# Kernel optimization log

Hardware: AMD Instinct MI355X
Metric: run time of the kernel (lower is better)

## Reference

```python
import jax, jax.numpy as jnp
import numpy as np

B, T, D, H = 4, 2048, 1024, 16
HD = D // H


def setup_inputs() -> dict:
    key = jax.random.key(0)
    ks = jax.random.split(key, 6)
    s = 0.02
    return {
        "x": jax.random.normal(ks[0], (B, T, D), dtype=jnp.float32),
        "padding_mask": jnp.zeros((B, T), dtype=bool),
        "Wq": jax.random.normal(ks[1], (D, D), dtype=jnp.float32) * s,
        "Wk": jax.random.normal(ks[2], (D, D), dtype=jnp.float32) * s,
        "Wv": jax.random.normal(ks[3], (D, D), dtype=jnp.float32) * s,
        "Wo": jax.random.normal(ks[4], (D, D), dtype=jnp.float32) * s,
        "bo": jax.random.normal(ks[5], (D,), dtype=jnp.float32) * s,
    }


def reference(x, padding_mask, Wq, Wk, Wv, Wo, bo):
    # torch nn.Linear: y = x @ W.T
    b, t, d = x.shape
    q = (x @ Wq.T).reshape(b, t, H, HD).transpose(0, 2, 1, 3)  # [B,H,T,hd]
    k = (x @ Wk.T).reshape(b, t, H, HD).transpose(0, 2, 1, 3)
    v = (x @ Wv.T).reshape(b, t, H, HD).transpose(0, 2, 1, 3)

    scores = jnp.einsum("bhid,bhjd->bhij", q, k) / jnp.sqrt(jnp.float32(HD))
    causal = jnp.tril(jnp.ones((t, t), dtype=bool))  # [T,T]
    neg_inf = jnp.float32(-jnp.inf)
    scores = jnp.where(causal[None, None, :, :], scores, neg_inf)
    scores = jnp.where(padding_mask[:, None, None, :], neg_inf, scores)

    attn = jax.nn.softmax(scores, axis=-1)
    out = jnp.einsum("bhij,bhjd->bhid", attn, v)
    out = out.transpose(0, 2, 1, 3).reshape(b, t, d)
    out = out @ Wo.T + bo
    nonpad = (~padding_mask)[:, :, None].astype(out.dtype)
    return out * nonpad
```

## Files before the change

### kernel.cpp

```cpp
#include <hip/hip_runtime.h>

#define B_ 4
#define T_ 2048
#define D_ 1024
#define H_ 16
#define BT_ (B_ * T_)
#define QSCALE (0.125f * 1.44269504088896f)

typedef unsigned short u16;
typedef __attribute__((ext_vector_type(8))) __bf16 bf16x8;
typedef __attribute__((ext_vector_type(4))) float f32x4;

__device__ __forceinline__ u16 f2bf(float f) {
  unsigned u = __builtin_bit_cast(unsigned, f);
  u += 0x7FFFu + ((u >> 16) & 1u);
  return (u16)(u >> 16);
}

__device__ __forceinline__ void gload16(const void* g, void* l) {
  __builtin_amdgcn_global_load_lds(
      (const __attribute__((address_space(1))) void*)g,
      (__attribute__((address_space(3))) void*)l, 16, 0, 0);
}

__global__ void cvt_bf16(const float* __restrict__ in, u16* __restrict__ out, int n4) {
  int i = blockIdx.x * 256 + threadIdx.x;
  if (i >= n4) return;
  const float4 v = ((const float4*)in)[i];
  ushort4 o;
  o.x = f2bf(v.x); o.y = f2bf(v.y); o.z = f2bf(v.z); o.w = f2bf(v.w);
  ((ushort4*)out)[i] = o;
}

__global__ void pm_flags(const unsigned char* __restrict__ pm, unsigned char* __restrict__ fl) {
  int i = threadIdx.x;
  const unsigned long long* p = (const unsigned long long*)(pm + i * 64);
  unsigned long long acc = 0;
#pragma unroll
  for (int k = 0; k < 8; ++k) acc |= p[k];
  fl[i] = acc ? 1 : 0;
}

template<int MODE>
__global__ __launch_bounds__(256, 2) void gemm_bt(
    const u16* __restrict__ A, const u16* __restrict__ Bw,
    float* __restrict__ Cf, const float* __restrict__ bias,
    const unsigned char* __restrict__ rowmask,
    u16* __restrict__ Cq, u16* __restrict__ Ck, u16* __restrict__ Cvt)
{
  __shared__ __align__(16) u16 sA[128 * 64];
  __shared__ __align__(16) u16 sB[128 * 64];
  const int tid = threadIdx.x;
  const int lane = tid & 63, wave = tid >> 6;
  const int g = lane >> 4, s15 = lane & 15;
  const int bm = blockIdx.x * 128, bn = blockIdx.y * 128;
  const int wr = wave >> 1, wc = wave & 1;

  const int srow = lane >> 3;
  const int scol = ((lane & 7) ^ srow) << 3;

  f32x4 acc[4][4] = {};

  for (int kt = 0; kt < 16; ++kt) {
    __syncthreads();
    const int k0 = kt << 6;
#pragma unroll
    for (int c = 0; c < 4; ++c) {
      const int chunk = c * 4 + wave;
      gload16(A  + (size_t)(bm + chunk * 8 + srow) * 1024 + k0 + scol, (char*)sA + chunk * 1024);
      gload16(Bw + (size_t)(bn + chunk * 8 + srow) * 1024 + k0 + scol, (char*)sB + chunk * 1024);
    }
    __syncthreads();
#pragma unroll
    for (int kk = 0; kk < 2; ++kk) {
      const int cb = ((kk << 6) | (g << 4)) ^ ((s15 & 7) << 4);
      bf16x8 af[4], bf[4];
#pragma unroll
      for (int mm = 0; mm < 4; ++mm)
        af[mm] = *(const bf16x8*)((const char*)sA + (wr * 64 + mm * 16 + s15) * 128 + cb);
#pragma unroll
      for (int nn = 0; nn < 4; ++nn)
        bf[nn] = *(const bf16x8*)((const char*)sB + (wc * 64 + nn * 16 + s15) * 128 + cb);
#pragma unroll
      for (int mm = 0; mm < 4; ++mm)
#pragma unroll
        for (int nn = 0; nn < 4; ++nn)
          acc[mm][nn] = __builtin_amdgcn_mfma_f32_16x16x32_bf16(af[mm], bf[nn], acc[mm][nn], 0, 0, 0);
    }
  }

  if (MODE == 1) {
    const int region = bn >> 10;
    const float a = (region == 0) ? QSCALE : 1.f;
#pragma unroll
    for (int mm = 0; mm < 4; ++mm)
#pragma unroll
      for (int nn = 0; nn < 4; ++nn) {
        const int col = bn + wc * 64 + nn * 16 + s15;
        const int colr = col & 1023;
        const int row0 = bm + wr * 64 + mm * 16 + (g << 2);
        if (region == 2) {
          ushort4 w;
          w.x = f2bf(acc[mm][nn][0]); w.y = f2bf(acc[mm][nn][1]);
          w.z = f2bf(acc[mm][nn][2]); w.w = f2bf(acc[mm][nn][3]);
          *(ushort4*)(Cvt + (size_t)colr * BT_ + row0) = w;
        } else {
          u16* dst = region ? Ck : Cq;
#pragma unroll
          for (int r = 0; r < 4; ++r)
            dst[(size_t)(row0 + r) * 1024 + colr] = f2bf(acc[mm][nn][r] * a);
        }
      }
  } else {
#pragma unroll
    for (int mm = 0; mm < 4; ++mm)
#pragma unroll
      for (int nn = 0; nn < 4; ++nn) {
        const int col = bn + wc * 64 + nn * 16 + s15;
        const int row0 = bm + wr * 64 + mm * 16 + (g << 2);
        const float bv = bias[col];
#pragma unroll
        for (int r = 0; r < 4; ++r) {
          float v = acc[mm][nn][r] + bv;
          v = rowmask[row0 + r] ? 0.f : v;
          Cf[(size_t)(row0 + r) * 1024 + col] = v;
        }
      }
  }
}

__global__ __launch_bounds__(512, 4) void attn_fwd(
    const u16* __restrict__ Q, const u16* __restrict__ K,
    const u16* __restrict__ VT, const unsigned char* __restrict__ pm,
    const unsigned char* __restrict__ tileflag, u16* __restrict__ O)
{
  __shared__ __align__(16) u16 sK[2][64 * 64];
  __shared__ __align__(16) u16 sV[2][64 * 64];
  const int tid = threadIdx.x;
  const int lane = tid & 63, wave = tid >> 6;
  const int g = lane >> 4, s15 = lane & 15;
  const int bh = blockIdx.x, b = bh >> 4, h = bh & 15;
  const int jpair = blockIdx.y;
  const size_t tokbase = (size_t)b * T_;

  const int srow = tid >> 3;
  const int sc = (tid & 7) ^ (srow & 7);
  const u16* Kb0 = K + tokbase * D_ + h * 64 + sc * 8;
  const u16* Vb0 = VT + (size_t)(h * 64) * BT_ + tokbase + sc * 8;

#pragma unroll
  for (int half = 0; half < 2; ++half) {
    const int qt = half ? (15 - jpair) : jpair;
    const int q0 = qt * 128;
    const int qw = q0 + wave * 16;
    const int nt = 2 * qt + 2;

    bf16x8 qf[2];
#pragma unroll
    for (int ks = 0; ks < 2; ++ks)
      qf[ks] = *(const bf16x8*)(Q + (tokbase + qw + s15) * D_ + h * 64 + ks * 32 + g * 8);

    f32x4 o[4] = {};
    float m_ = -1e30f, l_ = 0.f;

    gload16(Kb0 + (size_t)srow * D_,  (char*)(&sK[0][0]) + tid * 16);
    gload16(Vb0 + (size_t)srow * BT_, (char*)(&sV[0][0]) + tid * 16);
    __syncthreads();

    for (int t = 0; t < nt; ++t) {
      const int kv0 = t << 6;
      if (t + 1 < nt) {
        const int nb = (t + 1) & 1;
        gload16(Kb0 + (size_t)(kv0 + 64 + srow) * D_,  (char*)(&sK[nb][0]) + tid * 16);
        gload16(Vb0 + (size_t)srow * BT_ + kv0 + 64,   (char*)(&sV[nb][0]) + tid * 16);
      }

      if (kv0 <= qw + 15) {
        const u16* kb_ = &sK[t & 1][0];
        const u16* vb_ = &sV[t & 1][0];

        f32x4 st[4] = {};
#pragma unroll
        for (int ks = 0; ks < 2; ++ks) {
          bf16x8 kf[4];
#pragma unroll
          for (int jf = 0; jf < 4; ++jf)
            kf[jf] = *(const bf16x8*)(kb_ + (jf * 16 + s15) * 64 + (((ks * 4 + g) ^ (s15 & 7)) << 3));
          __builtin_amdgcn_s_setprio(1);
#pragma unroll
          for (int jf = 0; jf < 4; ++jf)
            st[jf] = __builtin_amdgcn_mfma_f32_16x16x32_bf16(kf[jf], qf[ks], st[jf], 0, 0, 0);
          __builtin_amdgcn_s_setprio(0);
        }

        if (kv0 + 63 > qw) {
          const int iq = qw + s15;
#pragma unroll
          for (int jf = 0; jf < 4; ++jf) {
            const int jb = kv0 + jf * 16 + g * 4;
#pragma unroll
            for (int r = 0; r < 4; ++r)
              if (jb + r > iq) st[jf][r] = -1e30f;
          }
        }
        if (tileflag[b * 32 + t]) {
#pragma unroll
          for (int jf = 0; jf < 4; ++jf) {
            const int jb = kv0 + jf * 16 + g * 4;
            uchar4 p4 = *(const uchar4*)(pm + b * T_ + jb);
            const unsigned char* pr = (const unsigned char*)&p4;
#pragma unroll
            for (int r = 0; r < 4; ++r)
              if (pr[r]) st[jf][r] = -1e30f;
          }
        }

        float tm = -1e30f;
#pragma unroll
        for (int jf = 0; jf < 4; ++jf)
          tm = fmaxf(tm, fmaxf(fmaxf(st[jf][0], st[jf][1]), fmaxf(st[jf][2], st[jf][3])));
        tm = fmaxf(tm, __shfl_xor(tm, 16));
        tm = fmaxf(tm, __shfl_xor(tm, 32));
        if (!__all(tm <= m_ + 8.f)) {
          const float mn = fmaxf(m_, tm);
          const float ac = __builtin_amdgcn_exp2f(m_ - mn);
          m_ = mn;
          l_ *= ac;
#pragma unroll
          for (int df = 0; df < 4; ++df) o[df] *= ac;
        }
        float s = 0.f;
#pragma unroll
        for (int jf = 0; jf < 4; ++jf)
#pragma unroll
          for (int r = 0; r < 4; ++r) {
            const float p = __builtin_amdgcn_exp2f(st[jf][r] - m_);
            st[jf][r] = p;
            s += p;
          }
        s += __shfl_xor(s, 16);
        s += __shfl_xor(s, 32);
        l_ += s;

#pragma unroll
        for (int kb2 = 0; kb2 < 2; ++kb2) {
          bf16x8 vf[4];
#pragma unroll
          for (int df = 0; df < 4; ++df)
            vf[df] = *(const bf16x8*)(vb_ + (df * 16 + s15) * 64 + (((kb2 * 4 + g) ^ (s15 & 7)) << 3));
          unsigned w00, w01, w10, w11;
          asm("v_cvt_pk_bf16_f32 %0, %1, %2" : "=v"(w00) : "v"(st[2*kb2][0]),   "v"(st[2*kb2][1]));
          asm("v_cvt_pk_bf16_f32 %0, %1, %2" : "=v"(w01) : "v"(st[2*kb2][2]),   "v"(st[2*kb2][3]));
          asm("v_cvt_pk_bf16_f32 %0, %1, %2" : "=v"(w10) : "v"(st[2*kb2+1][0]), "v"(st[2*kb2+1][1]));
          asm("v_cvt_pk_bf16_f32 %0, %1, %2" : "=v"(w11) : "v"(st[2*kb2+1][2]), "v"(st[2*kb2+1][3]));
          asm("v_permlane32_swap_b32 %0, %1" : "+v"(w00), "+v"(w10));
          asm("v_permlane16_swap_b32 %0, %1" : "+v"(w00), "+v"(w10));
          asm("v_permlane32_swap_b32 %0, %1" : "+v"(w01), "+v"(w11));
          asm("v_permlane16_swap_b32 %0, %1" : "+v"(w01), "+v"(w11));
          union { unsigned u[4]; bf16x8 v; } pf;
          pf.u[0] = w00; pf.u[1] = w01; pf.u[2] = w10; pf.u[3] = w11;
          __builtin_amdgcn_s_setprio(1);
#pragma unroll
          for (int df = 0; df < 4; ++df)
            o[df] = __builtin_amdgcn_mfma_f32_16x16x32_bf16(vf[df], pf.v, o[df], 0, 0, 0);
          __builtin_amdgcn_s_setprio(0);
        }
      }
      __syncthreads();
    }

    const float inv = 1.f / l_;
    u16* orow = O + (tokbase + qw + s15) * D_ + h * 64 + g * 4;
#pragma unroll
    for (int df = 0; df < 4; ++df) {
      ushort4 w;
      w.x = f2bf(o[df][0] * inv); w.y = f2bf(o[df][1] * inv);
      w.z = f2bf(o[df][2] * inv); w.w = f2bf(o[df][3] * inv);
      *(ushort4*)(orow + df * 16) = w;
    }
  }
}

extern "C" void kernel_launch(void* const* d_in, const int* in_sizes, int n_in,
                              void* d_out, int out_size, void* d_ws, size_t ws_size,
                              hipStream_t stream)
{
  const float* x  = (const float*)d_in[0];
  const unsigned char* pm = (const unsigned char*)d_in[1];
  const float* Wq = (const float*)d_in[2];
  const float* Wk = (const float*)d_in[3];
  const float* Wv = (const float*)d_in[4];
  const float* Wo = (const float*)d_in[5];
  const float* bo = (const float*)d_in[6];
  float* out = (float*)d_out;

  char* w = (char*)d_ws;
  u16* xb  = (u16*)w; w += (size_t)BT_ * D_ * 2;
  u16* wqb = (u16*)w; w += (size_t)D_ * D_ * 2;
  u16* wkb = (u16*)w; w += (size_t)D_ * D_ * 2;
  u16* wvb = (u16*)w; w += (size_t)D_ * D_ * 2;
  u16* wob = (u16*)w; w += (size_t)D_ * D_ * 2;
  u16* qb  = (u16*)w; w += (size_t)BT_ * D_ * 2;
  u16* kbf = (u16*)w; w += (size_t)BT_ * D_ * 2;
  u16* vt  = (u16*)w; w += (size_t)BT_ * D_ * 2;
  u16* ao  = (u16*)w; w += (size_t)BT_ * D_ * 2;
  unsigned char* flags = (unsigned char*)w; w += 256;

  const int nx4 = BT_ * D_ / 4;
  const int nw4 = D_ * D_ / 4;
  cvt_bf16<<<nx4 / 256, 256, 0, stream>>>(x, xb, nx4);
  cvt_bf16<<<nw4 / 256, 256, 0, stream>>>(Wq, wqb, nw4);
  cvt_bf16<<<nw4 / 256, 256, 0, stream>>>(Wk, wkb, nw4);
  cvt_bf16<<<nw4 / 256, 256, 0, stream>>>(Wv, wvb, nw4);
  cvt_bf16<<<nw4 / 256, 256, 0, stream>>>(Wo, wob, nw4);
  pm_flags<<<1, 128, 0, stream>>>(pm, flags);

  gemm_bt<1><<<dim3(64, 24), 256, 0, stream>>>(xb, wqb, nullptr, nullptr, nullptr, qb, kbf, vt);

  attn_fwd<<<dim3(B_ * H_, 8), 512, 0, stream>>>(qb, kbf, vt, pm, flags, ao);

  gemm_bt<0><<<dim3(64, 8), 256, 0, stream>>>(ao, wob, out, bo, pm, nullptr, nullptr, nullptr);
}
```

Baseline: 159.3 us.

## Rewrite QKV projection GEMM with 256x128 tiles, double-buffered LDS, and block swizzle

Replaces the templated QKV GEMM with a dedicated kernel that uses 512-thread blocks computing 256x128 tiles. Global-to-LDS loads for the next k-step are double-buffered so they overlap with the MFMA work on the current buffer. It also adds a flattened grid swizzle for L2 locality and raises wave priority around the MFMA block. The output projection keeps the old single-buffer kernel. The costs are twice the LDS footprint and extra barriers inside the k loop.

```diff
diff --git a/kernel.cpp b/kernel.cpp
--- a/kernel.cpp
+++ b/kernel.cpp
@@ -41,12 +41,106 @@
   fl[i] = acc ? 1 : 0;
 }
 
-template<int MODE>
-__global__ __launch_bounds__(256, 2) void gemm_bt(
+__global__ __launch_bounds__(512, 2) void gemm_qkv(
+    const u16* __restrict__ A, const u16* __restrict__ Bw,
+    u16* __restrict__ Cq, u16* __restrict__ Ck, u16* __restrict__ Cvt)
+{
+  __shared__ __align__(16) u16 sA[2][256 * 64];
+  __shared__ __align__(16) u16 sB[2][128 * 64];
+  const int tid = threadIdx.x;
+  const int lane = tid & 63, wave = tid >> 6;
+  const int g = lane >> 4, s15 = lane & 15;
+  const int wm = wave >> 1, wn = wave & 1;
+
+  const int flat = blockIdx.x;
+  const int swz = (flat & 7) * 96 + (flat >> 3);
+  const int bm = (swz / 24) * 256, bn = (swz % 24) * 128;
+
+  int rowL[2], offL[2];
+#pragma unroll
+  for (int l = 0; l < 2; ++l) {
+    const int chunk = tid + l * 512;
+    rowL[l] = chunk >> 3;
+    offL[l] = rowL[l] * 1024 + (((chunk & 7) ^ (rowL[l] & 7)) << 3);
+  }
+  const int ldsW = wave * 1024;
+
+  auto STAGE = [&](int t, int buf) {
+    const int k0 = t << 6;
+#pragma unroll
+    for (int h = 0; h < 2; ++h)
+#pragma unroll
+      for (int l = 0; l < 2; ++l)
+        gload16(A + (size_t)(bm + h * 128) * 1024 + k0 + offL[l],
+                (char*)&sA[buf][0] + h * 16384 + l * 8192 + ldsW);
+#pragma unroll
+    for (int l = 0; l < 2; ++l)
+      gload16(Bw + (size_t)bn * 1024 + k0 + offL[l],
+              (char*)&sB[buf][0] + l * 8192 + ldsW);
+  };
+
+  f32x4 acc[4][4] = {};
+
+  STAGE(0, 0);
+  asm volatile("s_waitcnt vmcnt(0)" ::: "memory");
+  __builtin_amdgcn_s_barrier();
+
+  for (int t = 0; t < 16; ++t) {
+    const int cur = t & 1;
+    const char* sa = (const char*)&sA[cur][0] + (wm >> 1) * 16384 + ((wm & 1) * 64) * 128;
+    const char* sb = (const char*)&sB[cur][0] + (wn * 64) * 128;
+    if (t < 15) STAGE(t + 1, cur ^ 1);
+#pragma unroll
+    for (int kk = 0; kk < 2; ++kk) {
+      const int cb = ((kk * 4 + g) ^ (s15 & 7)) << 4;
+      bf16x8 af[4], bf[4];
+#pragma unroll
+      for (int m = 0; m < 4; ++m)
+        af[m] = *(const bf16x8*)(sa + (m * 16 + s15) * 128 + cb);
+#pragma unroll
+      for (int n = 0; n < 4; ++n)
+        bf[n] = *(const bf16x8*)(sb + (n * 16 + s15) * 128 + cb);
+      __builtin_amdgcn_s_barrier();
+      __builtin_amdgcn_s_setprio(1);
+#pragma unroll
+      for (int m = 0; m < 4; ++m)
+#pragma unroll
+        for (int n = 0; n < 4; ++n)
+          acc[m][n] = __builtin_amdgcn_mfma_f32_16x16x32_bf16(af[m], bf[n], acc[m][n], 0, 0, 0);
+      __builtin_amdgcn_s_setprio(0);
+      if (kk == 0) __builtin_amdgcn_s_barrier();
+    }
+    if (t < 15) asm volatile("s_waitcnt vmcnt(0)" ::: "memory");
+    __builtin_amdgcn_s_barrier();
+  }
+
+  const int region = bn >> 10;
+  const float a = (region == 0) ? QSCALE : 1.f;
+#pragma unroll
+  for (int m = 0; m < 4; ++m)
+#pragma unroll
+    for (int n = 0; n < 4; ++n) {
+      const int col = bn + wn * 64 + n * 16 + s15;
+      const int colr = col & 1023;
+      const int row0 = bm + wm * 64 + m * 16 + (g << 2);
+      if (region == 2) {
+        ushort4 w;
+        w.x = f2bf(acc[m][n][0]); w.y = f2bf(acc[m][n][1]);
+        w.z = f2bf(acc[m][n][2]); w.w = f2bf(acc[m][n][3]);
+        *(ushort4*)(Cvt + (size_t)colr * BT_ + row0) = w;
+      } else {
+        u16* dst = region ? Ck : Cq;
+#pragma unroll
+        for (int r = 0; r < 4; ++r)
+          dst[(size_t)(row0 + r) * 1024 + colr] = f2bf(acc[m][n][r] * a);
+      }
+    }
+}
+
+__global__ __launch_bounds__(256, 2) void gemm_out(
     const u16* __restrict__ A, const u16* __restrict__ Bw,
     float* __restrict__ Cf, const float* __restrict__ bias,
-    const unsigned char* __restrict__ rowmask,
-    u16* __restrict__ Cq, u16* __restrict__ Ck, u16* __restrict__ Cvt)
+    const unsigned char* __restrict__ rowmask)
 {
   __shared__ __align__(16) u16 sA[128 * 64];
   __shared__ __align__(16) u16 sB[128 * 64];
@@ -89,44 +183,20 @@
     }
   }
 
-  if (MODE == 1) {
-    const int region = bn >> 10;
-    const float a = (region == 0) ? QSCALE : 1.f;
-#pragma unroll
-    for (int mm = 0; mm < 4; ++mm)
-#pragma unroll
-      for (int nn = 0; nn < 4; ++nn) {
-        const int col = bn + wc * 64 + nn * 16 + s15;
-        const int colr = col & 1023;
-        const int row0 = bm + wr * 64 + mm * 16 + (g << 2);
-        if (region == 2) {
-          ushort4 w;
-          w.x = f2bf(acc[mm][nn][0]); w.y = f2bf(acc[mm][nn][1]);
-          w.z = f2bf(acc[mm][nn][2]); w.w = f2bf(acc[mm][nn][3]);
-          *(ushort4*)(Cvt + (size_t)colr * BT_ + row0) = w;
-        } else {
-          u16* dst = region ? Ck : Cq;
-#pragma unroll
-          for (int r = 0; r < 4; ++r)
-            dst[(size_t)(row0 + r) * 1024 + colr] = f2bf(acc[mm][nn][r] * a);
-        }
+#pragma unroll
+  for (int mm = 0; mm < 4; ++mm)
+#pragma unroll
+    for (int nn = 0; nn < 4; ++nn) {
+      const int col = bn + wc * 64 + nn * 16 + s15;
+      const int row0 = bm + wr * 64 + mm * 16 + (g << 2);
+      const float bv = bias[col];
+#pragma unroll
+      for (int r = 0; r < 4; ++r) {
+        float v = acc[mm][nn][r] + bv;
+        v = rowmask[row0 + r] ? 0.f : v;
+        Cf[(size_t)(row0 + r) * 1024 + col] = v;
       }
-  } else {
-#pragma unroll
-    for (int mm = 0; mm < 4; ++mm)
-#pragma unroll
-      for (int nn = 0; nn < 4; ++nn) {
-        const int col = bn + wc * 64 + nn * 16 + s15;
-        const int row0 = bm + wr * 64 + mm * 16 + (g << 2);
-        const float bv = bias[col];
-#pragma unroll
-        for (int r = 0; r < 4; ++r) {
-          float v = acc[mm][nn][r] + bv;
-          v = rowmask[row0 + r] ? 0.f : v;
-          Cf[(size_t)(row0 + r) * 1024 + col] = v;
-        }
-      }
-  }
+    }
 }
 
 __global__ __launch_bounds__(512, 4) void attn_fwd(
@@ -315,9 +385,9 @@
   cvt_bf16<<<nw4 / 256, 256, 0, stream>>>(Wo, wob, nw4);
   pm_flags<<<1, 128, 0, stream>>>(pm, flags);
 
-  gemm_bt<1><<<dim3(64, 24), 256, 0, stream>>>(xb, wqb, nullptr, nullptr, nullptr, qb, kbf, vt);
+  gemm_qkv<<<768, 512, 0, stream>>>(xb, wqb, qb, kbf, vt);
 
   attn_fwd<<<dim3(B_ * H_, 8), 512, 0, stream>>>(qb, kbf, vt, pm, flags, ao);
 
-  gemm_bt<0><<<dim3(64, 8), 256, 0, stream>>>(ao, wob, out, bo, pm, nullptr, nullptr, nullptr);
-}
+  gemm_out<<<dim3(64, 8), 256, 0, stream>>>(ao, wob, out, bo, pm);
+}
```

Measured after the change: 189.3 us. +18.8%, slower.
